# Performance work log

Measured on AMD Instinct MI355X. Metric: run time of the kernel, lower is better.

Reference implementation:

```python
import jax, jax.numpy as jnp
import numpy as np

N_NODES = 100000
N_EDGES = 1600000
N_GRAPHS = 64
F = 50
N_LAYERS = 3
EPS_STD = 1e-5
EPS_BN = 1e-5


def _glorot(key, shape):
    fan_in, fan_out = shape[0], shape[1]
    lim = float(np.sqrt(6.0 / (fan_in + fan_out)))
    return jax.random.uniform(key, shape, jnp.float32, -lim, lim)


def setup_inputs() -> dict:
    key = jax.random.key(0)
    ks = jax.random.split(key, 20)
    x = jax.random.normal(ks[0], (N_NODES, 2), jnp.float32)
    edge_index = jax.random.randint(ks[1], (2, N_EDGES), 0, N_NODES, jnp.int32)
    batch_ids = jnp.sort(jax.random.randint(ks[2], (N_NODES,), 0, N_GRAPHS, jnp.int32))
    inp = {
        "x": x,
        "edge_index": edge_index,
        "batch_ids": batch_ids,
        "W_gcn": _glorot(ks[3], (2, F)),
        "b_gcn": jnp.zeros((F,), jnp.float32),
        # stacked per-layer PNA params [L, ...]
        "pre_W": jnp.stack([_glorot(jax.random.fold_in(ks[4], i), (2 * F, F)) for i in range(N_LAYERS)]),
        "pre_b": jnp.zeros((N_LAYERS, F), jnp.float32),
        "post_W": jnp.stack([_glorot(jax.random.fold_in(ks[5], i), (13 * F, F)) for i in range(N_LAYERS)]),
        "post_b": jnp.zeros((N_LAYERS, F), jnp.float32),
        "lin_W": jnp.stack([_glorot(jax.random.fold_in(ks[6], i), (F, F)) for i in range(N_LAYERS)]),
        "lin_b": jnp.zeros((N_LAYERS, F), jnp.float32),
        "bn_gamma": jnp.ones((N_LAYERS, F), jnp.float32),
        "bn_beta": jnp.zeros((N_LAYERS, F), jnp.float32),
        "mlp_W1": _glorot(ks[7], (F, 25)),
        "mlp_b1": jnp.zeros((25,), jnp.float32),
        "mlp_W2": _glorot(ks[8], (25, 1)),
        "mlp_b2": jnp.zeros((1,), jnp.float32),
    }
    return inp


def _pna_layer(x, src, dst, deg_raw, deg_c, avg_log, Wp, bp, Wq, bq, Wl, bl):
    # pre-NN on messages: concat(x_i, x_j) -> F   (i = target/dst, j = source/src)
    h = jnp.concatenate([x[dst], x[src]], axis=-1) @ Wp + bp  # [E, F]
    dc = deg_c[:, None]
    s = jax.ops.segment_sum(h, dst, num_segments=N_NODES)
    mean = s / dc
    mean_sq = jax.ops.segment_sum(h * h, dst, num_segments=N_NODES) / dc
    var = jax.nn.relu(mean_sq - mean * mean)
    std = jnp.sqrt(var + EPS_STD)
    has_edge = (deg_raw > 0)[:, None]
    mn = jnp.where(has_edge, jax.ops.segment_min(h, dst, num_segments=N_NODES), 0.0)
    mx = jnp.where(has_edge, jax.ops.segment_max(h, dst, num_segments=N_NODES), 0.0)
    agg = jnp.concatenate([mean, mn, mx, std], axis=-1)  # [N, 4F]
    amp = (jnp.log1p(deg_c) / avg_log)[:, None]
    att = (avg_log / jnp.log1p(deg_c))[:, None]
    out = jnp.concatenate([agg, agg * amp, agg * att], axis=-1)  # [N, 12F]
    out = jnp.concatenate([x, out], axis=-1) @ Wq + bq  # post-NN: [N, 13F] -> F
    return out @ Wl + bl


def reference(x, edge_index, batch_ids, W_gcn, b_gcn, pre_W, pre_b, post_W, post_b,
              lin_W, lin_b, bn_gamma, bn_beta, mlp_W1, mlp_b1, mlp_W2, mlp_b2):
    src, dst = edge_index[0], edge_index[1]

    # ---- GCNConv(2 -> 50) with self loops + symmetric normalization ----
    h = x @ W_gcn
    loop = jnp.arange(N_NODES, dtype=src.dtype)
    src_a = jnp.concatenate([src, loop])
    dst_a = jnp.concatenate([dst, loop])
    deg_sl = jax.ops.segment_sum(jnp.ones_like(src_a, jnp.float32), dst_a, num_segments=N_NODES)
    dinv = jnp.where(deg_sl > 0, jax.lax.rsqrt(deg_sl), 0.0)
    norm = (dinv[src_a] * dinv[dst_a])[:, None]
    h = jax.ops.segment_sum(h[src_a] * norm, dst_a, num_segments=N_NODES) + b_gcn

    # ---- degree stats for PNA scalers ----
    deg_raw = jax.ops.segment_sum(jnp.ones_like(src, jnp.float32), dst, num_segments=N_NODES)
    deg_c = jnp.maximum(deg_raw, 1.0)
    avg_log = jnp.mean(jnp.log1p(deg_raw))

    for l in range(N_LAYERS):
        h = _pna_layer(h, src, dst, deg_raw, deg_c, avg_log,
                       pre_W[l], pre_b[l], post_W[l], post_b[l], lin_W[l], lin_b[l])
        mu = jnp.mean(h, axis=0)
        var = jnp.mean((h - mu) ** 2, axis=0)
        h = (h - mu) * jax.lax.rsqrt(var + EPS_BN) * bn_gamma[l] + bn_beta[l]
        h = jax.nn.relu(h)

    # ---- global add pool + MLP (dropout is identity at eval) ----
    g = jax.ops.segment_sum(h, batch_ids, num_segments=N_GRAPHS)  # [G, F]
    g = jax.nn.relu(g @ mlp_W1 + mlp_b1)
    g = g @ mlp_W2 + mlp_b2  # [G, 1]
    return g.reshape(N_GRAPHS)
```

## Files before the change

### kernel.cpp

```cpp
#include <hip/hip_runtime.h>
#include <math.h>

#define NN 100000
#define NE 1600000
#define NG 64
#define FF 50
#define NL 3
#define NBUCK ((NN + 255) / 256)
#define CAP 8192

typedef short bf16x8 __attribute__((ext_vector_type(8)));
typedef float f32x4 __attribute__((ext_vector_type(4)));

__device__ __forceinline__ short f2bf(float f) {
  return __builtin_bit_cast(short, (__bf16)f);
}
__device__ __forceinline__ float bf2f(short s) {
  unsigned int u = ((unsigned int)(unsigned short)s) << 16;
  return __builtin_bit_cast(float, u);
}
__device__ __forceinline__ float2 unpk2(unsigned u) {
  float2 v;
  v.x = __builtin_bit_cast(float, u << 16);
  v.y = __builtin_bit_cast(float, u & 0xFFFF0000u);
  return v;
}
__device__ __forceinline__ unsigned pk2(float2 v) {
  return (unsigned)(unsigned short)f2bf(v.x) | ((unsigned)(unsigned short)f2bf(v.y) << 16);
}

__device__ __forceinline__ bf16x8 ldfrag_bn(const short* base, const float2* __restrict__ ab, int kbase) {
  bf16x8 raw = *(const bf16x8*)base;
  unsigned u[4];
  __builtin_memcpy(u, &raw, 16);
  short t[8] __attribute__((aligned(16)));
#pragma unroll
  for (int i = 0; i < 4; ++i) {
    float2 v = unpk2(u[i]);
    float2 a0 = ab[kbase + 2 * i], a1 = ab[kbase + 2 * i + 1];
    v.x = fmaxf(fmaf(v.x, a0.x, a0.y), 0.f);
    v.y = fmaxf(fmaf(v.y, a1.x, a1.y), 0.f);
    ((unsigned*)t)[i] = pk2(v);
  }
  bf16x8 r;
  __builtin_memcpy(&r, t, 16);
  return r;
}

__global__ __launch_bounds__(256) void k_bucket2(const int* __restrict__ src, const int* __restrict__ dst,
                                                 int* __restrict__ bcnt, unsigned* __restrict__ tmp) {
  __shared__ int hist[NBUCK];
  __shared__ int base[NBUCK];
  int t = threadIdx.x;
  for (int i = t; i < NBUCK; i += 256) hist[i] = 0;
  __syncthreads();
  int e0 = blockIdx.x * 4096;
  int myb[16], myrank[16];
  unsigned mypack[16];
#pragma unroll
  for (int i = 0; i < 16; ++i) {
    int e = e0 + i * 256 + t;
    if (e < NE) {
      int s = src[e], d = dst[e];
      int b = d >> 8;
      myb[i] = b;
      mypack[i] = ((unsigned)(d & 255) << 17) | (unsigned)s;
      myrank[i] = atomicAdd(&hist[b], 1);
    } else myb[i] = -1;
  }
  __syncthreads();
  for (int i = t; i < NBUCK; i += 256)
    base[i] = hist[i] ? atomicAdd(&bcnt[i], hist[i]) : 0;
  __syncthreads();
#pragma unroll
  for (int i = 0; i < 16; ++i)
    if (myb[i] >= 0) {
      int pos = base[myb[i]] + myrank[i];
      if (pos < CAP) tmp[(size_t)myb[i] * CAP + pos] = mypack[i];
    }
}

__global__ void k_bscan(const int* __restrict__ bcnt, int* __restrict__ bbase, int* __restrict__ off) {
  __shared__ int sm[512];
  int t = threadIdx.x;
  int v = (t < NBUCK) ? bcnt[t] : 0;
  sm[t] = v;
  __syncthreads();
  for (int o = 1; o < 512; o <<= 1) {
    int u = (t >= o) ? sm[t - o] : 0;
    __syncthreads();
    sm[t] += u;
    __syncthreads();
  }
  if (t < NBUCK) bbase[t] = sm[t] - v;
  if (t == 0) off[NN] = NE;
}

__global__ __launch_bounds__(256) void k_bsort2(const unsigned* __restrict__ tmp, const int* __restrict__ bcnt,
                                                const int* __restrict__ bbase, int* __restrict__ off,
                                                int* __restrict__ ssrc, float* __restrict__ dinv,
                                                float* __restrict__ lgc, float* __restrict__ scal) {
  __shared__ unsigned seg[CAP];
  __shared__ int loc[256];
  __shared__ int wred[4];
  __shared__ float fred[4];
  int b = blockIdx.x, t = threadIdx.x;
  int c = bcnt[b];
  if (c > CAP) c = CAP;
  int base = bbase[b];
  const unsigned* sp = tmp + (size_t)b * CAP;
  loc[t] = 0;
  __syncthreads();
  for (int e = t; e < c; e += 256) {
    unsigned p = sp[e];
    seg[e] = p;
    atomicAdd(&loc[p >> 17], 1);
  }
  __syncthreads();
  int d = loc[t];
  int lane = t & 63, w = t >> 6;
  int v = d;
#pragma unroll
  for (int o = 1; o < 64; o <<= 1) {
    int u = __shfl_up(v, o);
    if (lane >= o) v += u;
  }
  if (lane == 63) wred[w] = v;
  int n = b * 256 + t;
  float lp = (n < NN) ? log1pf((float)d) : 0.f;
#pragma unroll
  for (int o = 32; o > 0; o >>= 1) lp += __shfl_down(lp, o);
  if (lane == 0) fred[w] = lp;
  __syncthreads();
  int excl = v - d;
#pragma unroll
  for (int i = 0; i < 4; ++i)
    if (i < w) excl += wred[i];
  if (t == 0) atomicAdd(scal, fred[0] + fred[1] + fred[2] + fred[3]);
  if (n < NN) {
    off[n] = base + excl;
    dinv[n] = rsqrtf((float)(d + 1));
    lgc[n] = log1pf((float)(d > 1 ? d : 1));
  }
  loc[t] = base + excl;
  __syncthreads();
  for (int e = t; e < c; e += 256) {
    unsigned p = seg[e];
    int pos = atomicAdd(&loc[p >> 17], 1);
    ssrc[pos] = (int)(p & 0x1FFFFu);
  }
}

__global__ void k_fusew(const float* __restrict__ postW, const float* __restrict__ postb,
                        const float* __restrict__ linW, const float* __restrict__ linb,
                        float* __restrict__ A, float* __restrict__ bias2) {
  int wid = (blockIdx.x * blockDim.x + threadIdx.x) >> 6;
  int f = threadIdx.x & 63;
  if (wid >= 3 * 651) return;
  int l = wid / 651, r = wid % 651;
  int fc = f < FF ? f : FF - 1;
  const float* lw = linW + l * FF * FF;
  float acc = 0.f;
  if (r < 650) {
    const float* pw = postW + (l * 650 + r) * FF;
    for (int j = 0; j < FF; ++j) acc += pw[j] * lw[j * FF + fc];
    if (f < FF) A[(l * 650 + r) * FF + f] = acc;
  } else {
    const float* pb = postb + l * FF;
    for (int j = 0; j < FF; ++j) acc += pb[j] * lw[j * FF + fc];
    bias2[l * 64 + f] = (f < FF) ? (acc + linb[l * FF + f]) : 0.f;
  }
}

__global__ void k_packA(const float* __restrict__ Af, short* __restrict__ Abt) {
  int t = blockIdx.x * 256 + threadIdx.x;
  if (t >= 3 * 13 * 64 * 64) return;
  int kk = t & 63;
  int f = (t >> 6) & 63;
  int lc = t >> 12;
  int c = lc % 13;
  int l = lc / 13;
  float v = 0.f;
  if (kk < FF && f < FF) v = Af[((size_t)(l * 650 + c * FF + kk)) * FF + f];
  Abt[t] = f2bf(v);
}

__global__ void k_packP(const float* __restrict__ preW, short* __restrict__ Pbt) {
  int t = blockIdx.x * 256 + threadIdx.x;
  if (t >= NL * 2 * 64 * 64) return;
  int kk = t & 63;
  int f = (t >> 6) & 63;
  int ls = t >> 12;
  int s = ls & 1, l = ls >> 1;
  float v = 0.f;
  if (kk < FF && f < FF) v = preW[(size_t)(l * 100 + s * FF + kk) * FF + f];
  Pbt[t] = f2bf(v);
}

__global__ void k_gcnpre(const float* __restrict__ x, const float* __restrict__ Wg,
                         const float* __restrict__ dinv, short* __restrict__ pb) {
  int t = blockIdx.x * 256 + threadIdx.x;
  int n = t >> 6, f = t & 63;
  if (n >= NN) return;
  float v = 0.f;
  if (f < FF) v = (x[2 * n] * Wg[f] + x[2 * n + 1] * Wg[FF + f]) * dinv[n];
  pb[n * 64 + f] = f2bf(v);
}

__global__ void k_gcnagg(const short* __restrict__ pb, const int* __restrict__ off,
                         const int* __restrict__ ssrc, const float* __restrict__ dinv,
                         const float* __restrict__ bg, short* __restrict__ hb) {
  int wid = (blockIdx.x * blockDim.x + threadIdx.x) >> 6;
  int lane = threadIdx.x & 63;
  if (wid >= NN) return;
  int n = wid;
  float acc = bf2f(pb[(size_t)n * 64 + lane]);
  int lo = off[n], hi = off[n + 1];
  for (int base = lo; base < hi; base += 64) {
    int rem = hi - base;
    int cnt = rem > 64 ? 64 : rem;
    int sidx = (base + lane < hi) ? ssrc[base + lane] : 0;
    int k = 0;
    for (; k + 16 <= cnt; k += 16) {
      float v[16];
#pragma unroll
      for (int i = 0; i < 16; ++i) {
        int s = __builtin_amdgcn_readlane(sidx, k + i);
        v[i] = bf2f(pb[(size_t)s * 64 + lane]);
      }
#pragma unroll
      for (int i = 0; i < 16; ++i) acc += v[i];
    }
    if (k < cnt) {
      float v[16];
      int m = cnt - k;
#pragma unroll
      for (int i = 0; i < 16; ++i) {
        int kk = k + (i < m ? i : 0);
        int s = __builtin_amdgcn_readlane(sidx, kk);
        v[i] = bf2f(pb[(size_t)s * 64 + lane]);
      }
#pragma unroll
      for (int i = 0; i < 16; ++i)
        if (i < m) acc += v[i];
    }
  }
  float o = 0.f;
  if (lane < FF) o = dinv[n] * acc + bg[lane];
  hb[(size_t)n * 64 + lane] = f2bf(o);
}

__global__ __launch_bounds__(256) void k_preM(const short* __restrict__ hin, const float2* __restrict__ ab,
                                              const short* __restrict__ Pbt, const float* __restrict__ preb,
                                              short* __restrict__ cbh, short* __restrict__ bbh, int l) {
  int tid = threadIdx.x;
  int w = tid >> 6, lane = tid & 63;
  int q = lane >> 4, m16 = lane & 15;
  int n0 = blockIdx.x * 64 + w * 16;
  int anode = n0 + m16;
  int nsafe = anode < NN ? anode : 0;
  bf16x8 afr[2];
#pragma unroll
  for (int hh = 0; hh < 2; ++hh) {
    const short* srcp = hin + (size_t)nsafe * 64 + hh * 32 + q * 8;
    afr[hh] = ab ? ldfrag_bn(srcp, ab, hh * 32 + q * 8) : *(const bf16x8*)srcp;
  }
  const short* P0 = Pbt + l * 8192;
  f32x4 aT[4], aB2[4];
#pragma unroll
  for (int ft = 0; ft < 4; ++ft) {
    aT[ft] = (f32x4){0.f, 0.f, 0.f, 0.f};
    aB2[ft] = (f32x4){0.f, 0.f, 0.f, 0.f};
  }
#pragma unroll
  for (int hh = 0; hh < 2; ++hh) {
#pragma unroll
    for (int ft = 0; ft < 4; ++ft) {
      bf16x8 b0 = *(const bf16x8*)(P0 + ((ft * 16 + m16) << 6) + hh * 32 + q * 8);
      bf16x8 b1 = *(const bf16x8*)(P0 + 4096 + ((ft * 16 + m16) << 6) + hh * 32 + q * 8);
      aT[ft] = __builtin_amdgcn_mfma_f32_16x16x32_bf16(afr[hh], b0, aT[ft], 0, 0, 0);
      aB2[ft] = __builtin_amdgcn_mfma_f32_16x16x32_bf16(afr[hh], b1, aB2[ft], 0, 0, 0);
    }
  }
#pragma unroll
  for (int r = 0; r < 4; ++r) {
    int node = n0 + q * 4 + r;
    if (node >= NN) continue;
#pragma unroll
    for (int ft = 0; ft < 4; ++ft) {
      int col = ft * 16 + m16;
      cbh[node * 64 + col] = (col < FF) ? f2bf(aT[ft][r] + preb[l * FF + col]) : 0;
      bbh[node * 64 + col] = f2bf(aB2[ft][r]);
    }
  }
}

__global__ void k_agg(const short* __restrict__ bbh, const short* __restrict__ cbh,
                      const int* __restrict__ off, const int* __restrict__ ssrc,
                      const float* __restrict__ lgc, const float* __restrict__ scal,
                      short* __restrict__ agb, float* __restrict__ ampatt) {
  int wid = (blockIdx.x * blockDim.x + threadIdx.x) >> 6;
  int lane = threadIdx.x & 63;
  if (wid >= NN) return;
  int n = wid;
  float S = 0.f, S2 = 0.f;
  float MN = INFINITY, MX = -INFINITY;
  int lo = off[n], hi = off[n + 1];
  for (int base = lo; base < hi; base += 64) {
    int rem = hi - base;
    int cnt = rem > 64 ? 64 : rem;
    int sidx = (base + lane < hi) ? ssrc[base + lane] : 0;
    int k = 0;
    for (; k + 16 <= cnt; k += 16) {
      float v[16];
#pragma unroll
      for (int i = 0; i < 16; ++i) {
        int s = __builtin_amdgcn_readlane(sidx, k + i);
        v[i] = bf2f(bbh[(size_t)s * 64 + lane]);
      }
#pragma unroll
      for (int i = 0; i < 16; ++i) {
        float x = v[i];
        S += x;
        S2 = fmaf(x, x, S2);
        MN = fminf(MN, x);
        MX = fmaxf(MX, x);
      }
    }
    if (k < cnt) {
      float v[16];
      int m = cnt - k;
#pragma unroll
      for (int i = 0; i < 16; ++i) {
        int kk = k + (i < m ? i : 0);
        int s = __builtin_amdgcn_readlane(sidx, kk);
        v[i] = bf2f(bbh[(size_t)s * 64 + lane]);
      }
#pragma unroll
      for (int i = 0; i < 16; ++i) {
        if (i < m) {
          float x = v[i];
          S += x;
          S2 = fmaf(x, x, S2);
          MN = fminf(MN, x);
          MX = fmaxf(MX, x);
        }
      }
    }
  }
  int d = hi - lo;
  bool valid = lane < FF;
  float mean, mnv, mxv, stdv;
  if (d > 0) {
    float inv = 1.f / (float)d;
    float m = S * inv;
    float vv = S2 * inv - m * m; vv = vv > 0.f ? vv : 0.f;
    stdv = sqrtf(vv + 1e-5f);
    float c = valid ? bf2f(cbh[(size_t)n * 64 + lane]) : 0.f;
    mean = c + m;
    mnv = c + MN;
    mxv = c + MX;
  } else {
    mean = mnv = mxv = 0.f;
    stdv = sqrtf(1e-5f);
  }
  short* row = agb + (size_t)n * 256;
  row[lane]       = valid ? f2bf(mean) : 0;
  row[64 + lane]  = valid ? f2bf(mnv) : 0;
  row[128 + lane] = valid ? f2bf(mxv) : 0;
  row[192 + lane] = valid ? f2bf(stdv) : 0;
  if (lane == 0) {
    float avg = scal[0] * (1.f / NN);
    float lg = lgc[n];
    ampatt[2 * n] = lg / avg;
    ampatt[2 * n + 1] = avg / lg;
  }
}

__global__ __launch_bounds__(512, 2) void k_gemm(const short* __restrict__ h, const float2* __restrict__ ab,
                                                 const short* __restrict__ agb, const float* __restrict__ ampatt,
                                                 const short* __restrict__ Abt, const float* __restrict__ bias2,
                                                 short* __restrict__ hout, float* __restrict__ bnsumR) {
  __shared__ short Bs[3][64][72];
  int tid = threadIdx.x;
  int w = tid >> 6, lane = tid & 63;
  int q = lane >> 4, m16 = lane & 15;
  int n0 = blockIdx.x * 128 + w * 16;

  int anode = n0 + m16;
  int nsafe = anode < NN ? anode : 0;
  bf16x8 afr[5][2];
  {
#pragma unroll
    for (int hh = 0; hh < 2; ++hh) {
      const short* srcp = h + (size_t)nsafe * 64 + hh * 32 + q * 8;
      afr[0][hh] = ab ? ldfrag_bn(srcp, ab, hh * 32 + q * 8) : *(const bf16x8*)srcp;
    }
    const short* arow = agb + (size_t)nsafe * 256;
#pragma unroll
    for (int c = 1; c <= 4; ++c)
#pragma unroll
      for (int hh = 0; hh < 2; ++hh)
        afr[c][hh] = *(const bf16x8*)(arow + (c - 1) * 64 + hh * 32 + q * 8);
  }

  f32x4 acc[3][4];
#pragma unroll
  for (int s = 0; s < 3; ++s)
#pragma unroll
    for (int ft = 0; ft < 4; ++ft) acc[s][ft] = (f32x4){0.f, 0.f, 0.f, 0.f};

  bool stager = tid < 256;
  int bf = tid >> 2;
  int bko = (tid & 3) * 16;
  float4 rg[3][2];
  if (stager) {
    const float4* g = (const float4*)(Abt + (bf << 6) + bko);
    rg[0][0] = g[0]; rg[0][1] = g[1];
  }
  for (int ph = 0; ph < 5; ++ph) {
    int nslice = (ph == 0) ? 1 : 3;
    if (ph) __syncthreads();
    if (stager) {
      for (int s = 0; s < nslice; ++s) {
        *(float4*)&Bs[s][bf][bko] = rg[s][0];
        *(float4*)&Bs[s][bf][bko + 8] = rg[s][1];
      }
    }
    __syncthreads();
    if (stager && ph < 4) {
#pragma unroll
      for (int s = 0; s < 3; ++s) {
        int chunk = (ph + 1) + 4 * s;
        const float4* g = (const float4*)(Abt + (chunk << 12) + (bf << 6) + bko);
        rg[s][0] = g[0]; rg[s][1] = g[1];
      }
    }
    if (ph == 0) {
#pragma unroll
      for (int hh = 0; hh < 2; ++hh)
#pragma unroll
        for (int ft = 0; ft < 4; ++ft) {
          bf16x8 b = *(const bf16x8*)&Bs[0][ft * 16 + m16][hh * 32 + q * 8];
          acc[0][ft] = __builtin_amdgcn_mfma_f32_16x16x32_bf16(afr[0][hh], b, acc[0][ft], 0, 0, 0);
        }
    } else {
#pragma unroll
      for (int hh = 0; hh < 2; ++hh)
#pragma unroll
        for (int s = 0; s < 3; ++s)
#pragma unroll
          for (int ft = 0; ft < 4; ++ft) {
            bf16x8 b = *(const bf16x8*)&Bs[s][ft * 16 + m16][hh * 32 + q * 8];
            acc[s][ft] = __builtin_amdgcn_mfma_f32_16x16x32_bf16(afr[ph][hh], b, acc[s][ft], 0, 0, 0);
          }
    }
  }

  float sacc[4] = {0.f, 0.f, 0.f, 0.f};
  float qacc[4] = {0.f, 0.f, 0.f, 0.f};
#pragma unroll
  for (int r = 0; r < 4; ++r) {
    int node = n0 + q * 4 + r;
    if (node >= NN) continue;
    float2 aa = *(const float2*)(ampatt + 2 * node);
#pragma unroll
    for (int ft = 0; ft < 4; ++ft) {
      int col = ft * 16 + m16;
      float val = 0.f;
      if (col < FF) {
        val = acc[0][ft][r] + aa.x * acc[1][ft][r] + aa.y * acc[2][ft][r] + bias2[col];
        sacc[ft] += val;
        qacc[ft] = fmaf(val, val, qacc[ft]);
      }
      hout[node * 64 + col] = f2bf(val);
    }
  }
#pragma unroll
  for (int ft = 0; ft < 4; ++ft) {
    sacc[ft] += __shfl_xor(sacc[ft], 16);
    sacc[ft] += __shfl_xor(sacc[ft], 32);
    qacc[ft] += __shfl_xor(qacc[ft], 16);
    qacc[ft] += __shfl_xor(qacc[ft], 32);
  }
  __syncthreads();
  float* red = (float*)&Bs[0][0][0];
  if (lane < 16) {
#pragma unroll
    for (int ft = 0; ft < 4; ++ft) {
      red[w * 128 + ft * 16 + lane]      = sacc[ft];
      red[w * 128 + 64 + ft * 16 + lane] = qacc[ft];
    }
  }
  __syncthreads();
  if (tid < 128) {
    float v = 0.f;
#pragma unroll
    for (int i = 0; i < 8; ++i) v += red[i * 128 + tid];
    atomicAdd(&bnsumR[(blockIdx.x & 7) * 128 + tid], v);
  }
}

__global__ void k_bnab(const float* __restrict__ bnsumR, const float* __restrict__ gamma,
                       const float* __restrict__ beta, float2* __restrict__ ab, int l) {
  int f = threadIdx.x;
  float a = 0.f, b = 0.f;
  if (f < FF) {
    float s = 0.f, q = 0.f;
    for (int r = 0; r < 8; ++r) { s += bnsumR[r * 128 + f]; q += bnsumR[r * 128 + 64 + f]; }
    float mu = s * (1.f / NN);
    float vq = q * (1.f / NN) - mu * mu;
    float rs = rsqrtf((vq > 0.f ? vq : 0.f) + 1e-5f);
    a = rs * gamma[l * FF + f];
    b = beta[l * FF + f] - mu * a;
  }
  ab[f] = make_float2(a, b);
}

__global__ void k_gsum(const short* __restrict__ h, const float2* __restrict__ ab,
                       const int* __restrict__ batch, float* __restrict__ gsum) {
  int w = threadIdx.x >> 6, lane = threadIdx.x & 63;
  int fc = lane < FF ? lane : FF - 1;
  bool act = lane < FF;
  float2 p = ab[fc];
  int n0 = blockIdx.x * 256 + w * 64;
  if (n0 >= NN) return;
  int nEnd = n0 + 64 < NN ? n0 + 64 : NN;
  float acc = 0.f;
  int gcur = batch[n0];
  for (int n = n0; n < nEnd; ++n) {
    int g = batch[n];
    if (g != gcur) {
      if (act) atomicAdd(&gsum[gcur * 64 + lane], acc);
      acc = 0.f; gcur = g;
    }
    float v = bf2f(h[n * 64 + fc]);
    acc += fmaxf(fmaf(v, p.x, p.y), 0.f);
  }
  if (act) atomicAdd(&gsum[gcur * 64 + lane], acc);
}

__global__ void k_mlp(const float* __restrict__ gsum, const float* __restrict__ W1,
                      const float* __restrict__ b1, const float* __restrict__ W2,
                      const float* __restrict__ b2, float* __restrict__ out) {
  int g = threadIdx.x;
  if (g >= NG) return;
  float gv[FF];
#pragma unroll
  for (int f = 0; f < FF; ++f) gv[f] = gsum[g * 64 + f];
  float r = b2[0];
  for (int j = 0; j < 25; ++j) {
    float a = b1[j];
#pragma unroll
    for (int f = 0; f < FF; ++f) a = fmaf(gv[f], W1[f * 25 + j], a);
    r += fmaxf(a, 0.f) * W2[j];
  }
  out[g] = r;
}

extern "C" void kernel_launch(void* const* d_in, const int* in_sizes, int n_in,
                              void* d_out, int out_size, void* d_ws, size_t ws_size,
                              hipStream_t stream) {
  const float* x     = (const float*)d_in[0];
  const int*   ei    = (const int*)d_in[1];
  const int*   src   = ei;
  const int*   dst   = ei + NE;
  const int*   batch = (const int*)d_in[2];
  const float* Wg    = (const float*)d_in[3];
  const float* bg    = (const float*)d_in[4];
  const float* preW  = (const float*)d_in[5];
  const float* preb  = (const float*)d_in[6];
  const float* postW = (const float*)d_in[7];
  const float* postb = (const float*)d_in[8];
  const float* linW  = (const float*)d_in[9];
  const float* linb  = (const float*)d_in[10];
  const float* gamma = (const float*)d_in[11];
  const float* beta  = (const float*)d_in[12];
  const float* W1    = (const float*)d_in[13];
  const float* b1    = (const float*)d_in[14];
  const float* W2    = (const float*)d_in[15];
  const float* b2    = (const float*)d_in[16];
  float* out = (float*)d_out;

  char* W = (char*)d_ws;
  int*    bcnt   = (int*)(W + 0);
  int*    bbase  = (int*)(W + 2048);
  int*    off    = (int*)(W + 400384);
  float*  dinv   = (float*)(W + 807424);
  float*  lgc    = (float*)(W + 1207808);
  float*  scal   = (float*)(W + 1608192);
  float*  bnsum  = (float*)(W + 1608704);
  float2* ab     = (float2*)(W + 1620992);
  float*  Af     = (float*)(W + 1622528);
  float*  bias2  = (float*)(W + 2012672);
  short*  Abt    = (short*)(W + 2013696);
  short*  Pbt    = (short*)(W + 2333184);
  int*    ssrc   = (int*)(W + 8782336);
  short*  hA     = (short*)(W + 15182336);
  short*  hB     = (short*)(W + 27982592);
  short*  cbh    = (short*)(W + 40782848);
  short*  bbh    = (short*)(W + 53583104);
  short*  agb    = (short*)(W + 66383360);
  float*  ampatt = (float*)(W + 117583616);
  float*  gsum   = (float*)(W + 118383872);
  unsigned* tmp  = (unsigned*)agb;

  hipMemsetAsync(bcnt, 0, 2048, stream);
  hipMemsetAsync(scal, 0, 12800, stream);
  hipMemsetAsync(gsum, 0, 16384, stream);

  k_bucket2<<<(NE + 4095) / 4096, 256, 0, stream>>>(src, dst, bcnt, tmp);
  k_bscan<<<1, 512, 0, stream>>>(bcnt, bbase, off);
  k_bsort2<<<NBUCK, 256, 0, stream>>>(tmp, bcnt, bbase, off, ssrc, dinv, lgc, scal);
  k_fusew<<<(3 * 651 + 3) / 4, 256, 0, stream>>>(postW, postb, linW, linb, Af, bias2);
  k_packA<<<(3 * 13 * 64 * 64 + 255) / 256, 256, 0, stream>>>(Af, Abt);
  k_packP<<<(NL * 2 * 64 * 64 + 255) / 256, 256, 0, stream>>>(preW, Pbt);

  k_gcnpre<<<NN / 4, 256, 0, stream>>>(x, Wg, dinv, bbh);
  k_gcnagg<<<NN / 4, 256, 0, stream>>>(bbh, off, ssrc, dinv, bg, hA);

  short* hin = hA;
  short* hout = hB;
  for (int l = 0; l < NL; ++l) {
    const float2* abl = (l == 0) ? nullptr : (ab + (l - 1) * 64);
    k_preM<<<(NN + 63) / 64, 256, 0, stream>>>(hin, abl, Pbt, preb, cbh, bbh, l);
    k_agg<<<NN / 4, 256, 0, stream>>>(bbh, cbh, off, ssrc, lgc, scal, agb, ampatt);
    k_gemm<<<(NN + 127) / 128, 512, 0, stream>>>(hin, abl, agb, ampatt,
                                                 Abt + l * 13 * 4096, bias2 + l * 64, hout,
                                                 bnsum + l * 1024);
    k_bnab<<<1, 64, 0, stream>>>(bnsum + l * 1024, gamma, beta, ab + l * 64, l);
    short* t = hin; hin = hout; hout = t;
  }
  k_gsum<<<NBUCK, 256, 0, stream>>>(hin, ab + 2 * 64, batch, gsum);
  k_mlp<<<1, 64, 0, stream>>>(gsum, W1, b1, W2, b2, out);
}
```

Measured before the change: 655.6 us.

## Split gathered feature rows into two 32-column halves and gather in two phases

The per-node message buffers are stored as two separate 32-column planes instead of one 64-column row. The gather kernels run two phases, one per plane, with each half-wave taking alternate edges, and the halves are combined by a cross-lane shuffle. Each phase only touches a half-size array, which is meant to keep more of the gathered data resident in cache. In exchange the edge index list is walked twice, a block-wide barrier is added between phases, and the inner loop carries extra select and readlane work.

```diff
diff --git a/kernel.cpp b/kernel.cpp
--- a/kernel.cpp
+++ b/kernel.cpp
@@ -198,61 +198,74 @@
 }
 
 __global__ void k_gcnpre(const float* __restrict__ x, const float* __restrict__ Wg,
-                         const float* __restrict__ dinv, short* __restrict__ pb) {
+                         const float* __restrict__ dinv, short* __restrict__ pA,
+                         short* __restrict__ pB) {
   int t = blockIdx.x * 256 + threadIdx.x;
   int n = t >> 6, f = t & 63;
   if (n >= NN) return;
   float v = 0.f;
   if (f < FF) v = (x[2 * n] * Wg[f] + x[2 * n + 1] * Wg[FF + f]) * dinv[n];
-  pb[n * 64 + f] = f2bf(v);
-}
-
-__global__ void k_gcnagg(const short* __restrict__ pb, const int* __restrict__ off,
-                         const int* __restrict__ ssrc, const float* __restrict__ dinv,
-                         const float* __restrict__ bg, short* __restrict__ hb) {
+  short* dst = (f < 32) ? pA : pB;
+  dst[(n << 5) + (f & 31)] = f2bf(v);
+}
+
+__global__ void k_gcnagg(const short* __restrict__ pA, const short* __restrict__ pB,
+                         const int* __restrict__ off, const int* __restrict__ ssrc,
+                         const float* __restrict__ dinv, const float* __restrict__ bg,
+                         short* __restrict__ hb) {
   int wid = (blockIdx.x * blockDim.x + threadIdx.x) >> 6;
   int lane = threadIdx.x & 63;
   if (wid >= NN) return;
   int n = wid;
-  float acc = bf2f(pb[(size_t)n * 64 + lane]);
+  int hf = lane >> 5, fi = lane & 31;
   int lo = off[n], hi = off[n + 1];
-  for (int base = lo; base < hi; base += 64) {
-    int rem = hi - base;
-    int cnt = rem > 64 ? 64 : rem;
-    int sidx = (base + lane < hi) ? ssrc[base + lane] : 0;
-    int k = 0;
-    for (; k + 16 <= cnt; k += 16) {
-      float v[16];
-#pragma unroll
-      for (int i = 0; i < 16; ++i) {
-        int s = __builtin_amdgcn_readlane(sidx, k + i);
-        v[i] = bf2f(pb[(size_t)s * 64 + lane]);
-      }
-#pragma unroll
-      for (int i = 0; i < 16; ++i) acc += v[i];
-    }
-    if (k < cnt) {
-      float v[16];
-      int m = cnt - k;
-#pragma unroll
-      for (int i = 0; i < 16; ++i) {
-        int kk = k + (i < m ? i : 0);
-        int s = __builtin_amdgcn_readlane(sidx, kk);
-        v[i] = bf2f(pb[(size_t)s * 64 + lane]);
-      }
-#pragma unroll
-      for (int i = 0; i < 16; ++i)
-        if (i < m) acc += v[i];
-    }
-  }
-  float o = 0.f;
-  if (lane < FF) o = dinv[n] * acc + bg[lane];
-  hb[(size_t)n * 64 + lane] = f2bf(o);
+  float dv = dinv[n];
+#pragma unroll 1
+  for (int ph = 0; ph < 2; ++ph) {
+    const short* P = ph ? pB : pA;
+    float acc = (hf == 0) ? bf2f(P[(n << 5) + fi]) : 0.f;
+    for (int base = lo; base < hi; base += 64) {
+      int rem = hi - base;
+      int cnt = rem > 64 ? 64 : rem;
+      int sidx = (base + lane < hi) ? ssrc[base + lane] : 0;
+      int k = 0;
+      for (; k + 16 <= cnt; k += 16) {
+        float v[8];
+#pragma unroll
+        for (int i = 0; i < 8; ++i) {
+          int sA = __builtin_amdgcn_readlane(sidx, k + 2 * i);
+          int sB = __builtin_amdgcn_readlane(sidx, k + 2 * i + 1);
+          int s = hf ? sB : sA;
+          v[i] = bf2f(P[(s << 5) + fi]);
+        }
+#pragma unroll
+        for (int i = 0; i < 8; ++i) acc += v[i];
+      }
+      for (; k + 2 <= cnt; k += 2) {
+        int sA = __builtin_amdgcn_readlane(sidx, k);
+        int sB = __builtin_amdgcn_readlane(sidx, k + 1);
+        int s = hf ? sB : sA;
+        acc += bf2f(P[(s << 5) + fi]);
+      }
+      if (k < cnt) {
+        int sA = __builtin_amdgcn_readlane(sidx, cnt - 1);
+        if (hf == 0) acc += bf2f(P[(sA << 5) + fi]);
+      }
+    }
+    acc += __shfl_xor(acc, 32);
+    if (lane < 32) {
+      int col = (ph << 5) + fi;
+      float o = (col < FF) ? (dv * acc + bg[col]) : 0.f;
+      hb[(size_t)n * 64 + col] = f2bf(o);
+    }
+    if (ph == 0) __syncthreads();
+  }
 }
 
 __global__ __launch_bounds__(256) void k_preM(const short* __restrict__ hin, const float2* __restrict__ ab,
                                               const short* __restrict__ Pbt, const float* __restrict__ preb,
-                                              short* __restrict__ cbh, short* __restrict__ bbh, int l) {
+                                              short* __restrict__ cbh, short* __restrict__ bbA,
+                                              short* __restrict__ bbB, int l) {
   int tid = threadIdx.x;
   int w = tid >> 6, lane = tid & 63;
   int q = lane >> 4, m16 = lane & 15;
@@ -290,12 +303,14 @@
     for (int ft = 0; ft < 4; ++ft) {
       int col = ft * 16 + m16;
       cbh[node * 64 + col] = (col < FF) ? f2bf(aT[ft][r] + preb[l * FF + col]) : 0;
-      bbh[node * 64 + col] = f2bf(aB2[ft][r]);
-    }
-  }
-}
-
-__global__ void k_agg(const short* __restrict__ bbh, const short* __restrict__ cbh,
+      short* dst = (ft < 2) ? bbA : bbB;
+      dst[(node << 5) + (col & 31)] = f2bf(aB2[ft][r]);
+    }
+  }
+}
+
+__global__ void k_agg(const short* __restrict__ bbA, const short* __restrict__ bbB,
+                      const short* __restrict__ cbh,
                       const int* __restrict__ off, const int* __restrict__ ssrc,
                       const float* __restrict__ lgc, const float* __restrict__ scal,
                       short* __restrict__ agb, float* __restrict__ ampatt) {
@@ -303,72 +318,78 @@
   int lane = threadIdx.x & 63;
   if (wid >= NN) return;
   int n = wid;
-  float S = 0.f, S2 = 0.f;
-  float MN = INFINITY, MX = -INFINITY;
+  int hf = lane >> 5, fi = lane & 31;
   int lo = off[n], hi = off[n + 1];
-  for (int base = lo; base < hi; base += 64) {
-    int rem = hi - base;
-    int cnt = rem > 64 ? 64 : rem;
-    int sidx = (base + lane < hi) ? ssrc[base + lane] : 0;
-    int k = 0;
-    for (; k + 16 <= cnt; k += 16) {
-      float v[16];
-#pragma unroll
-      for (int i = 0; i < 16; ++i) {
-        int s = __builtin_amdgcn_readlane(sidx, k + i);
-        v[i] = bf2f(bbh[(size_t)s * 64 + lane]);
-      }
-#pragma unroll
-      for (int i = 0; i < 16; ++i) {
-        float x = v[i];
-        S += x;
-        S2 = fmaf(x, x, S2);
-        MN = fminf(MN, x);
-        MX = fmaxf(MX, x);
-      }
-    }
-    if (k < cnt) {
-      float v[16];
-      int m = cnt - k;
-#pragma unroll
-      for (int i = 0; i < 16; ++i) {
-        int kk = k + (i < m ? i : 0);
-        int s = __builtin_amdgcn_readlane(sidx, kk);
-        v[i] = bf2f(bbh[(size_t)s * 64 + lane]);
-      }
-#pragma unroll
-      for (int i = 0; i < 16; ++i) {
-        if (i < m) {
+  int d = hi - lo;
+  short* row = agb + (size_t)n * 256;
+#pragma unroll 1
+  for (int ph = 0; ph < 2; ++ph) {
+    const short* B = ph ? bbB : bbA;
+    float S = 0.f, S2 = 0.f, MN = INFINITY, MX = -INFINITY;
+    for (int base = lo; base < hi; base += 64) {
+      int rem = hi - base;
+      int cnt = rem > 64 ? 64 : rem;
+      int sidx = (base + lane < hi) ? ssrc[base + lane] : 0;
+      int k = 0;
+      for (; k + 16 <= cnt; k += 16) {
+        float v[8];
+#pragma unroll
+        for (int i = 0; i < 8; ++i) {
+          int sA = __builtin_amdgcn_readlane(sidx, k + 2 * i);
+          int sB = __builtin_amdgcn_readlane(sidx, k + 2 * i + 1);
+          int s = hf ? sB : sA;
+          v[i] = bf2f(B[(s << 5) + fi]);
+        }
+#pragma unroll
+        for (int i = 0; i < 8; ++i) {
           float x = v[i];
-          S += x;
-          S2 = fmaf(x, x, S2);
-          MN = fminf(MN, x);
-          MX = fmaxf(MX, x);
+          S += x; S2 = fmaf(x, x, S2);
+          MN = fminf(MN, x); MX = fmaxf(MX, x);
         }
       }
-    }
-  }
-  int d = hi - lo;
-  bool valid = lane < FF;
-  float mean, mnv, mxv, stdv;
-  if (d > 0) {
-    float inv = 1.f / (float)d;
-    float m = S * inv;
-    float vv = S2 * inv - m * m; vv = vv > 0.f ? vv : 0.f;
-    stdv = sqrtf(vv + 1e-5f);
-    float c = valid ? bf2f(cbh[(size_t)n * 64 + lane]) : 0.f;
-    mean = c + m;
-    mnv = c + MN;
-    mxv = c + MX;
-  } else {
-    mean = mnv = mxv = 0.f;
-    stdv = sqrtf(1e-5f);
-  }
-  short* row = agb + (size_t)n * 256;
-  row[lane]       = valid ? f2bf(mean) : 0;
-  row[64 + lane]  = valid ? f2bf(mnv) : 0;
-  row[128 + lane] = valid ? f2bf(mxv) : 0;
-  row[192 + lane] = valid ? f2bf(stdv) : 0;
+      for (; k + 2 <= cnt; k += 2) {
+        int sA = __builtin_amdgcn_readlane(sidx, k);
+        int sB = __builtin_amdgcn_readlane(sidx, k + 1);
+        int s = hf ? sB : sA;
+        float x = bf2f(B[(s << 5) + fi]);
+        S += x; S2 = fmaf(x, x, S2);
+        MN = fminf(MN, x); MX = fmaxf(MX, x);
+      }
+      if (k < cnt) {
+        int sA = __builtin_amdgcn_readlane(sidx, cnt - 1);
+        if (hf == 0) {
+          float x = bf2f(B[(sA << 5) + fi]);
+          S += x; S2 = fmaf(x, x, S2);
+          MN = fminf(MN, x); MX = fmaxf(MX, x);
+        }
+      }
+    }
+    S += __shfl_xor(S, 32); S2 += __shfl_xor(S2, 32);
+    MN = fminf(MN, __shfl_xor(MN, 32)); MX = fmaxf(MX, __shfl_xor(MX, 32));
+    if (lane < 32) {
+      int col = (ph << 5) + fi;
+      bool valid = col < FF;
+      float mean, mnv, mxv, stdv;
+      if (d > 0) {
+        float inv = 1.f / (float)d;
+        float m = S * inv;
+        float vv = S2 * inv - m * m; vv = vv > 0.f ? vv : 0.f;
+        stdv = sqrtf(vv + 1e-5f);
+        float c = valid ? bf2f(cbh[(size_t)n * 64 + col]) : 0.f;
+        mean = c + m;
+        mnv = c + MN;
+        mxv = c + MX;
+      } else {
+        mean = mnv = mxv = 0.f;
+        stdv = sqrtf(1e-5f);
+      }
+      row[col]       = valid ? f2bf(mean) : 0;
+      row[64 + col]  = valid ? f2bf(mnv) : 0;
+      row[128 + col] = valid ? f2bf(mxv) : 0;
+      row[192 + col] = valid ? f2bf(stdv) : 0;
+    }
+    if (ph == 0) __syncthreads();
+  }
   if (lane == 0) {
     float avg = scal[0] * (1.f / NN);
     float lg = lgc[n];
@@ -603,6 +624,8 @@
   short*  agb    = (short*)(W + 66383360);
   float*  ampatt = (float*)(W + 117583616);
   float*  gsum   = (float*)(W + 118383872);
+  short*  bbA    = bbh;
+  short*  bbB    = bbh + (size_t)NN * 32;
   unsigned* tmp  = (unsigned*)agb;
 
   hipMemsetAsync(bcnt, 0, 2048, stream);
@@ -616,15 +639,15 @@
   k_packA<<<(3 * 13 * 64 * 64 + 255) / 256, 256, 0, stream>>>(Af, Abt);
   k_packP<<<(NL * 2 * 64 * 64 + 255) / 256, 256, 0, stream>>>(preW, Pbt);
 
-  k_gcnpre<<<NN / 4, 256, 0, stream>>>(x, Wg, dinv, bbh);
-  k_gcnagg<<<NN / 4, 256, 0, stream>>>(bbh, off, ssrc, dinv, bg, hA);
+  k_gcnpre<<<NN / 4, 256, 0, stream>>>(x, Wg, dinv, bbA, bbB);
+  k_gcnagg<<<NN / 4, 256, 0, stream>>>(bbA, bbB, off, ssrc, dinv, bg, hA);
 
   short* hin = hA;
   short* hout = hB;
   for (int l = 0; l < NL; ++l) {
     const float2* abl = (l == 0) ? nullptr : (ab + (l - 1) * 64);
-    k_preM<<<(NN + 63) / 64, 256, 0, stream>>>(hin, abl, Pbt, preb, cbh, bbh, l);
-    k_agg<<<NN / 4, 256, 0, stream>>>(bbh, cbh, off, ssrc, lgc, scal, agb, ampatt);
+    k_preM<<<(NN + 63) / 64, 256, 0, stream>>>(hin, abl, Pbt, preb, cbh, bbA, bbB, l);
+    k_agg<<<NN / 4, 256, 0, stream>>>(bbA, bbB, cbh, off, ssrc, lgc, scal, agb, ampatt);
     k_gemm<<<(NN + 127) / 128, 512, 0, stream>>>(hin, abl, agb, ampatt,
                                                  Abt + l * 13 * 4096, bias2 + l * 64, hout,
                                                  bnsum + l * 1024);
```

New measurement: 862.4 us. 1.32x slower.
